# Optimization experiments

Hardware: AMD Instinct MI355X
Metric: run time of the kernel (lower is better)

Reference implementation:

```python
import jax, jax.numpy as jnp
import numpy as np

N, E, IN_DIM, HID = 50000, 800000, 512, 256
EPS = 1e-5


def _gat_layer(x, W, a_src, a_dst, b, src, dst, n, heads, ch):
    # x: [N, F_in] -> h: [N, H, C]
    h = (x @ W).reshape(n, heads, ch)
    alpha_src = jnp.sum(h * a_src, axis=-1)  # [N, H]
    alpha_dst = jnp.sum(h * a_dst, axis=-1)  # [N, H]
    e = jax.nn.leaky_relu(alpha_src[src] + alpha_dst[dst], negative_slope=0.2)  # [E', H]
    # segment softmax over incoming edges of each destination node
    m = jax.ops.segment_max(e, dst, num_segments=n)  # [N, H]
    ex = jnp.exp(e - m[dst])
    den = jax.ops.segment_sum(ex, dst, num_segments=n)  # [N, H]
    alpha = ex / den[dst]
    out = jax.ops.segment_sum(alpha[:, :, None] * h[src], dst, num_segments=n)  # [N, H, C]
    return out.reshape(n, heads * ch) + b


def _layer_norm(x, w, b):
    mu = jnp.mean(x, axis=-1, keepdims=True)
    var = jnp.mean(jnp.square(x - mu), axis=-1, keepdims=True)
    return (x - mu) * jax.lax.rsqrt(var + EPS) * w + b


def setup_inputs() -> dict:
    key = jax.random.key(0)
    ks = jax.random.split(key, 16)
    d = {}
    d['x'] = jax.random.normal(ks[0], (N, IN_DIM), dtype=jnp.float32)
    d['edge_index'] = jax.random.randint(ks[1], (2, E), 0, N, dtype=jnp.int32)
    s = 0.05
    # layer 0: GATConv(512, 64, heads=4)
    d['W0'] = jax.random.normal(ks[2], (IN_DIM, HID), dtype=jnp.float32) * s
    d['as0'] = jax.random.normal(ks[3], (4, 64), dtype=jnp.float32) * s
    d['ad0'] = jax.random.normal(ks[4], (4, 64), dtype=jnp.float32) * s
    d['b0'] = jnp.zeros((HID,), dtype=jnp.float32)
    d['lnw0'] = jnp.ones((HID,), dtype=jnp.float32)
    d['lnb0'] = jnp.zeros((HID,), dtype=jnp.float32)
    # layer 1: GATConv(256, 64, heads=4)
    d['W1'] = jax.random.normal(ks[5], (HID, HID), dtype=jnp.float32) * s
    d['as1'] = jax.random.normal(ks[6], (4, 64), dtype=jnp.float32) * s
    d['ad1'] = jax.random.normal(ks[7], (4, 64), dtype=jnp.float32) * s
    d['b1'] = jnp.zeros((HID,), dtype=jnp.float32)
    d['lnw1'] = jnp.ones((HID,), dtype=jnp.float32)
    d['lnb1'] = jnp.zeros((HID,), dtype=jnp.float32)
    # layer 2: GATConv(256, 256, heads=1)
    d['W2'] = jax.random.normal(ks[8], (HID, HID), dtype=jnp.float32) * s
    d['as2'] = jax.random.normal(ks[9], (1, HID), dtype=jnp.float32) * s
    d['ad2'] = jax.random.normal(ks[10], (1, HID), dtype=jnp.float32) * s
    d['b2'] = jnp.zeros((HID,), dtype=jnp.float32)
    d['lnw2'] = jnp.ones((HID,), dtype=jnp.float32)
    d['lnb2'] = jnp.zeros((HID,), dtype=jnp.float32)
    return d


def reference(x, edge_index, W0, as0, ad0, b0, lnw0, lnb0,
              W1, as1, ad1, b1, lnw1, lnb1,
              W2, as2, ad2, b2, lnw2, lnb2):
    n = x.shape[0]
    loop = jnp.arange(n, dtype=edge_index.dtype)
    src = jnp.concatenate([edge_index[0], loop])  # PyG add_self_loops=True
    dst = jnp.concatenate([edge_index[1], loop])
    h = _gat_layer(x, W0, as0, ad0, b0, src, dst, n, 4, 64)
    h = jax.nn.elu(_layer_norm(h, lnw0, lnb0))
    h = _gat_layer(h, W1, as1, ad1, b1, src, dst, n, 4, 64)
    h = jax.nn.elu(_layer_norm(h, lnw1, lnb1))
    h = _gat_layer(h, W2, as2, ad2, b2, src, dst, n, 1, HID)
    h = jax.nn.elu(_layer_norm(h, lnw2, lnb2))
    return h
```

## Files before the change

### kernel.cpp

```cpp
#include <hip/hip_runtime.h>

#define HID 256
#define EPSV 1e-5f
#define ASTR 72
#define BSTR 40

typedef __bf16 bf16x8 __attribute__((ext_vector_type(8)));
typedef float  floatx4 __attribute__((ext_vector_type(4)));

static __device__ __forceinline__ ushort f2bf(float f) {
  union { float f; unsigned int i; } c; c.f = f;
  unsigned int u = c.i;
  u += 0x7FFFu + ((u >> 16) & 1u);
  return (ushort)(u >> 16);
}
static __device__ __forceinline__ float bf2f(ushort u) {
  union { unsigned int i; float f; } c; c.i = ((unsigned int)u) << 16; return c.f;
}

__global__ void count_kernel(const int* __restrict__ ei, int* __restrict__ deg, int E, int tot) {
  int i = blockIdx.x * blockDim.x + threadIdx.x;
  if (i < tot) {
    int dst = (i < E) ? ei[E + i] : (i - E);
    atomicAdd(&deg[dst], 1);
  }
}

__global__ void scanA_kernel(const int* __restrict__ deg, int* __restrict__ incl,
                             int* __restrict__ sums, int n) {
  __shared__ int buf[1024];
  const int t = threadIdx.x;
  const int i = blockIdx.x * 1024 + t;
  int x = (i < n) ? deg[i] : 0;
  buf[t] = x;
  __syncthreads();
  for (int off = 1; off < 1024; off <<= 1) {
    int v = (t >= off) ? buf[t - off] : 0;
    __syncthreads();
    buf[t] += v;
    __syncthreads();
  }
  if (i < n) incl[i] = buf[t];
  if (t == 1023) sums[blockIdx.x] = buf[1023];
}

__global__ void scanB_kernel(int* __restrict__ sums, int* __restrict__ offs, int nblk) {
  __shared__ int buf[256];
  const int t = threadIdx.x;
  int x = (t < nblk) ? sums[t] : 0;
  buf[t] = x;
  __syncthreads();
  for (int off = 1; off < 256; off <<= 1) {
    int v = (t >= off) ? buf[t - off] : 0;
    __syncthreads();
    buf[t] += v;
    __syncthreads();
  }
  if (t < nblk) offs[t] = buf[t] - x;
  if (t == nblk) offs[nblk] = buf[nblk - 1];
}

__global__ void scanC_kernel(const int* __restrict__ deg, const int* __restrict__ incl,
                             const int* __restrict__ offs, int* __restrict__ rp,
                             int* __restrict__ cur, int n, int nblk) {
  const int i = blockIdx.x * 1024 + threadIdx.x;
  if (i < n) {
    int v = offs[blockIdx.x] + incl[i] - deg[i];
    rp[i] = v;
    cur[i] = v;
  }
  if (i == 0) rp[n] = offs[nblk];
}

__global__ void scatter_kernel(const int* __restrict__ ei, int* __restrict__ cur,
                               int* __restrict__ csr, int E, int tot) {
  int i = blockIdx.x * blockDim.x + threadIdx.x;
  if (i < tot) {
    int src = (i < E) ? ei[i] : (i - E);
    int dst = (i < E) ? ei[E + i] : (i - E);
    int pos = atomicAdd(&cur[dst], 1);
    csr[pos] = src;
  }
}

__global__ void transpose_kernel(const float* __restrict__ W, ushort* __restrict__ Wt, int K) {
  int i = blockIdx.x * blockDim.x + threadIdx.x;
  if (i < K * 256) {
    int k = i >> 8, m = i & 255;
    Wt[m * K + k] = f2bf(W[i]);
  }
}

static __device__ __forceinline__ void alpha_epilogue(
    const floatx4 (&acc)[4][4], const float* __restrict__ avs,
    const float* __restrict__ avd, float* __restrict__ asrc,
    float* __restrict__ adst, int row0, int col0, int wm, int wn,
    int quad, int m16, int H, int nrows) {
  float sv[4], dv[4];
  #pragma unroll
  for (int j = 0; j < 4; j++) {
    int col = col0 + wn + j * 16 + m16;
    sv[j] = avs[col];
    dv[j] = avd[col];
  }
  const int hd = (col0 + wn) >> 6;
  #pragma unroll
  for (int i = 0; i < 4; i++) {
    #pragma unroll
    for (int r = 0; r < 4; r++) {
      int row = row0 + wm + i * 16 + quad * 4 + r;
      float s = 0.f, d = 0.f;
      #pragma unroll
      for (int j = 0; j < 4; j++) {
        s = fmaf(acc[i][j][r], sv[j], s);
        d = fmaf(acc[i][j][r], dv[j], d);
      }
      #pragma unroll
      for (int o = 1; o < 16; o <<= 1) { s += __shfl_xor(s, o); d += __shfl_xor(d, o); }
      if (m16 == 0 && row < nrows) {
        if (H == 4) {
          asrc[row * 4 + hd] = s;
          adst[row * 4 + hd] = d;
        } else {
          atomicAdd(&asrc[row], s);
          atomicAdd(&adst[row], d);
        }
      }
    }
  }
}

__global__ __launch_bounds__(256) void gemm_kernel(
    const float* __restrict__ A, const ushort* __restrict__ Bt,
    ushort* __restrict__ hb, const float* __restrict__ avs,
    const float* __restrict__ avd, float* __restrict__ asrc,
    float* __restrict__ adst, int nrows, int K) {
  __shared__ ushort At[128 * ASTR];
  __shared__ ushort Bs[128 * BSTR];
  const int tid  = threadIdx.x;
  const int lane = tid & 63;
  const int wave = tid >> 6;
  const int quad = lane >> 4;
  const int m16  = lane & 15;
  const int row0 = blockIdx.x * 128;
  const int col0 = blockIdx.y * 128;
  const int wm = (wave >> 1) * 64;
  const int wn = (wave & 1) * 64;

  floatx4 acc[4][4];
  #pragma unroll
  for (int i = 0; i < 4; i++)
    #pragma unroll
    for (int j = 0; j < 4; j++) acc[i][j] = (floatx4){0.f, 0.f, 0.f, 0.f};

  const int arow = tid >> 3;
  const int acol = (tid & 7) * 4;
  const int brow = tid >> 2;
  const int bcol = (tid & 3) * 8;

  for (int k0 = 0; k0 < K; k0 += 32) {
    #pragma unroll
    for (int i = 0; i < 4; i++) {
      int r = arow + 32 * i;
      int ar = min(row0 + r, nrows - 1);
      floatx4 v = *(const floatx4*)(A + (size_t)ar * K + k0 + acol);
      union { ushort us[4]; unsigned long long u64; } ph, pl;
      #pragma unroll
      for (int j = 0; j < 4; j++) {
        ushort hi = f2bf(v[j]);
        ph.us[j] = hi;
        pl.us[j] = f2bf(v[j] - bf2f(hi));
      }
      *(unsigned long long*)&At[r * ASTR + acol]      = ph.u64;
      *(unsigned long long*)&At[r * ASTR + 32 + acol] = pl.u64;
    }
    #pragma unroll
    for (int i = 0; i < 2; i++) {
      int r = brow + 64 * i;
      *(int4*)&Bs[r * BSTR + bcol] =
          *(const int4*)(Bt + (size_t)(col0 + r) * K + k0 + bcol);
    }
    __syncthreads();
    bf16x8 bfr[4];
    #pragma unroll
    for (int j = 0; j < 4; j++)
      bfr[j] = *(const bf16x8*)&Bs[(wn + j * 16 + m16) * BSTR + quad * 8];
    #pragma unroll
    for (int p = 0; p < 2; p++) {
      bf16x8 af[4];
      #pragma unroll
      for (int i = 0; i < 4; i++)
        af[i] = *(const bf16x8*)&At[(wm + i * 16 + m16) * ASTR + p * 32 + quad * 8];
      #pragma unroll
      for (int i = 0; i < 4; i++)
        #pragma unroll
        for (int j = 0; j < 4; j++)
          acc[i][j] = __builtin_amdgcn_mfma_f32_16x16x32_bf16(af[i], bfr[j], acc[i][j], 0, 0, 0);
    }
    __syncthreads();
  }
  #pragma unroll
  for (int i = 0; i < 4; i++) {
    int rbase = row0 + wm + i * 16 + quad * 4;
    #pragma unroll
    for (int j = 0; j < 4; j++) {
      int col = col0 + wn + j * 16 + m16;
      #pragma unroll
      for (int r = 0; r < 4; r++) {
        int row = rbase + r;
        if (row < nrows) hb[(size_t)row * HID + col] = f2bf(acc[i][j][r]);
      }
    }
  }
  alpha_epilogue(acc, avs, avd, asrc, adst, row0, col0, wm, wn, quad, m16, 4, nrows);
}

__global__ __launch_bounds__(256) void gemm_packed_kernel(
    const ushort* __restrict__ A, const ushort* __restrict__ Bt,
    ushort* __restrict__ hb, const float* __restrict__ avs,
    const float* __restrict__ avd, float* __restrict__ asrc,
    float* __restrict__ adst, int nrows, int H) {
  __shared__ ushort At[128 * BSTR];
  __shared__ ushort Bs[128 * BSTR];
  const int tid  = threadIdx.x;
  const int lane = tid & 63;
  const int wave = tid >> 6;
  const int quad = lane >> 4;
  const int m16  = lane & 15;
  const int row0 = blockIdx.x * 128;
  const int col0 = blockIdx.y * 128;
  const int wm = (wave >> 1) * 64;
  const int wn = (wave & 1) * 64;

  floatx4 acc[4][4];
  #pragma unroll
  for (int i = 0; i < 4; i++)
    #pragma unroll
    for (int j = 0; j < 4; j++) acc[i][j] = (floatx4){0.f, 0.f, 0.f, 0.f};

  const int srow = tid >> 2;
  const int scol = (tid & 3) * 8;

  for (int k0 = 0; k0 < 512; k0 += 32) {
    const int kb = k0 & 255;
    #pragma unroll
    for (int i = 0; i < 2; i++) {
      int r = srow + 64 * i;
      int ar = min(row0 + r, nrows - 1);
      *(int4*)&At[r * BSTR + scol] = *(const int4*)(A + (size_t)ar * 512 + k0 + scol);
      *(int4*)&Bs[r * BSTR + scol] = *(const int4*)(Bt + (size_t)(col0 + r) * 256 + kb + scol);
    }
    __syncthreads();
    bf16x8 af[4], bfr[4];
    #pragma unroll
    for (int j = 0; j < 4; j++)
      bfr[j] = *(const bf16x8*)&Bs[(wn + j * 16 + m16) * BSTR + quad * 8];
    #pragma unroll
    for (int i = 0; i < 4; i++)
      af[i] = *(const bf16x8*)&At[(wm + i * 16 + m16) * BSTR + quad * 8];
    #pragma unroll
    for (int i = 0; i < 4; i++)
      #pragma unroll
      for (int j = 0; j < 4; j++)
        acc[i][j] = __builtin_amdgcn_mfma_f32_16x16x32_bf16(af[i], bfr[j], acc[i][j], 0, 0, 0);
    __syncthreads();
  }
  #pragma unroll
  for (int i = 0; i < 4; i++) {
    int rbase = row0 + wm + i * 16 + quad * 4;
    #pragma unroll
    for (int j = 0; j < 4; j++) {
      int col = col0 + wn + j * 16 + m16;
      #pragma unroll
      for (int r = 0; r < 4; r++) {
        int row = rbase + r;
        if (row < nrows) hb[(size_t)row * HID + col] = f2bf(acc[i][j][r]);
      }
    }
  }
  alpha_epilogue(acc, avs, avd, asrc, adst, row0, col0, wm, wn, quad, m16, H, nrows);
}

__global__ __launch_bounds__(256) void agg_ln_kernel(
    const ushort* __restrict__ hb, const float* __restrict__ asrc,
    const float* __restrict__ adst, const int* __restrict__ rp,
    const int* __restrict__ csr,
    const float* __restrict__ bias, const float* __restrict__ lnw,
    const float* __restrict__ lnb, ushort* __restrict__ apk,
    float* __restrict__ fout, int H, int n) {
  __shared__ float2 exs[4][64];
  const int t = threadIdx.x;
  const int w = t >> 6, lane = t & 63;
  const int nid = blockIdx.x * 4 + w;
  if (nid >= n) return;
  const int CH = (H == 4) ? 16 : 64;
  const int jj = lane & (CH - 1);
  const int hh = (H == 4) ? (lane >> 4) : 0;
  const int ch = 4 * lane;
  const float ad = adst[nid * H + hh];
  const int beg = rp[nid], end = rp[nid + 1];
  const char* hbase = (const char*)hb + ch * 2;
  float den = 0.f;
  float a0 = 0.f, a1 = 0.f, a2 = 0.f, a3 = 0.f;
  float b0 = 0.f, b1 = 0.f, b2 = 0.f, b3 = 0.f;
  float c0_ = 0.f, c1 = 0.f, c2 = 0.f, c3 = 0.f;
  float d0_ = 0.f, d1 = 0.f, d2 = 0.f, d3 = 0.f;

  int snext = 0;
  {
    int cnt0 = min(CH, end - beg);
    if (lane < cnt0) snext = csr[beg + lane];
  }

  for (int c0 = beg; c0 < end; c0 += CH) {
    const int cnt = min(CH, end - c0);
    int s = snext;
    const int nc0 = c0 + CH;
    if (nc0 < end) {
      int ncnt = min(CH, end - nc0);
      if (lane < ncnt) snext = csr[nc0 + lane];
    }
    s = __shfl(s, jj);
    float ex = 0.f;
    if (jj < cnt) {
      float e = asrc[s * H + hh] + ad;
      e = (e > 0.f) ? e : 0.2f * e;
      ex = __expf(fminf(e, 60.f));
    }
    exs[w][lane] = make_float2(ex, __int_as_float(s << 9));
    float dsum = ex;
    #pragma unroll
    for (int o = 32; o > 0; o >>= 1)
      if (o < CH) dsum += __shfl_xor(dsum, o);
    den += dsum;
    const float2* exw = &exs[w][hh * CH];
    int j = 0;
    for (; j + 4 <= cnt; j += 4) {
      float2 q0 = exw[j];
      float2 q1 = exw[j + 1];
      float2 q2 = exw[j + 2];
      float2 q3 = exw[j + 3];
      uint2 u0 = *(const uint2*)(hbase + __float_as_int(q0.y));
      uint2 u1 = *(const uint2*)(hbase + __float_as_int(q1.y));
      uint2 u2 = *(const uint2*)(hbase + __float_as_int(q2.y));
      uint2 u3 = *(const uint2*)(hbase + __float_as_int(q3.y));
      a0 = fmaf(q0.x, __uint_as_float(u0.x << 16), a0);
      a1 = fmaf(q0.x, __uint_as_float(u0.x & 0xffff0000u), a1);
      a2 = fmaf(q0.x, __uint_as_float(u0.y << 16), a2);
      a3 = fmaf(q0.x, __uint_as_float(u0.y & 0xffff0000u), a3);
      b0 = fmaf(q1.x, __uint_as_float(u1.x << 16), b0);
      b1 = fmaf(q1.x, __uint_as_float(u1.x & 0xffff0000u), b1);
      b2 = fmaf(q1.x, __uint_as_float(u1.y << 16), b2);
      b3 = fmaf(q1.x, __uint_as_float(u1.y & 0xffff0000u), b3);
      c0_ = fmaf(q2.x, __uint_as_float(u2.x << 16), c0_);
      c1 = fmaf(q2.x, __uint_as_float(u2.x & 0xffff0000u), c1);
      c2 = fmaf(q2.x, __uint_as_float(u2.y << 16), c2);
      c3 = fmaf(q2.x, __uint_as_float(u2.y & 0xffff0000u), c3);
      d0_ = fmaf(q3.x, __uint_as_float(u3.x << 16), d0_);
      d1 = fmaf(q3.x, __uint_as_float(u3.x & 0xffff0000u), d1);
      d2 = fmaf(q3.x, __uint_as_float(u3.y << 16), d2);
      d3 = fmaf(q3.x, __uint_as_float(u3.y & 0xffff0000u), d3);
    }
    for (; j < cnt; ++j) {
      float2 q0 = exw[j];
      uint2 u0 = *(const uint2*)(hbase + __float_as_int(q0.y));
      a0 = fmaf(q0.x, __uint_as_float(u0.x << 16), a0);
      a1 = fmaf(q0.x, __uint_as_float(u0.x & 0xffff0000u), a1);
      a2 = fmaf(q0.x, __uint_as_float(u0.y << 16), a2);
      a3 = fmaf(q0.x, __uint_as_float(u0.y & 0xffff0000u), a3);
    }
  }
  a0 += b0 + c0_ + d0_;
  a1 += b1 + c1 + d1;
  a2 += b2 + c2 + d2;
  a3 += b3 + c3 + d3;

  const float inv = 1.f / den;
  const floatx4 bia = *(const floatx4*)(bias + ch);
  float v0 = a0 * inv + bia[0];
  float v1 = a1 * inv + bia[1];
  float v2 = a2 * inv + bia[2];
  float v3 = a3 * inv + bia[3];
  float r1 = v0 + v1 + v2 + v3;
  #pragma unroll
  for (int o = 32; o > 0; o >>= 1) r1 += __shfl_xor(r1, o);
  float mu = r1 * (1.f / HID);
  float e0 = v0 - mu, e1 = v1 - mu, e2 = v2 - mu, e3 = v3 - mu;
  float r2 = e0 * e0 + e1 * e1 + e2 * e2 + e3 * e3;
  #pragma unroll
  for (int o = 32; o > 0; o >>= 1) r2 += __shfl_xor(r2, o);
  float rstd = rsqrtf(r2 * (1.f / HID) + EPSV);
  const floatx4 wv = *(const floatx4*)(lnw + ch);
  const floatx4 bv = *(const floatx4*)(lnb + ch);
  float y0 = e0 * rstd * wv[0] + bv[0];
  float y1 = e1 * rstd * wv[1] + bv[1];
  float y2 = e2 * rstd * wv[2] + bv[2];
  float y3 = e3 * rstd * wv[3] + bv[3];
  float o0 = (y0 > 0.f) ? y0 : expm1f(y0);
  float o1 = (y1 > 0.f) ? y1 : expm1f(y1);
  float o2 = (y2 > 0.f) ? y2 : expm1f(y2);
  float o3 = (y3 > 0.f) ? y3 : expm1f(y3);
  if (apk) {
    union { ushort us[4]; unsigned long long u64; } ph, pl;
    ushort h0 = f2bf(o0), h1 = f2bf(o1), h2 = f2bf(o2), h3 = f2bf(o3);
    ph.us[0] = h0; ph.us[1] = h1; ph.us[2] = h2; ph.us[3] = h3;
    pl.us[0] = f2bf(o0 - bf2f(h0)); pl.us[1] = f2bf(o1 - bf2f(h1));
    pl.us[2] = f2bf(o2 - bf2f(h2)); pl.us[3] = f2bf(o3 - bf2f(h3));
    *(unsigned long long*)(apk + (size_t)nid * 512 + ch)       = ph.u64;
    *(unsigned long long*)(apk + (size_t)nid * 512 + 256 + ch) = pl.u64;
  } else {
    floatx4 ov; ov[0] = o0; ov[1] = o1; ov[2] = o2; ov[3] = o3;
    *(floatx4*)(fout + (size_t)nid * HID + ch) = ov;
  }
}

extern "C" void kernel_launch(void* const* d_in, const int* in_sizes, int n_in,
                              void* d_out, int out_size, void* d_ws, size_t ws_size,
                              hipStream_t stream) {
  const float* x  = (const float*)d_in[0];
  const int*   ei = (const int*)d_in[1];
  const float* Wm[3]  = {(const float*)d_in[2], (const float*)d_in[8],  (const float*)d_in[14]};
  const float* Avs[3] = {(const float*)d_in[3], (const float*)d_in[9],  (const float*)d_in[15]};
  const float* Avd[3] = {(const float*)d_in[4], (const float*)d_in[10], (const float*)d_in[16]};
  const float* Bia[3] = {(const float*)d_in[5], (const float*)d_in[11], (const float*)d_in[17]};
  const float* Lnw[3] = {(const float*)d_in[6], (const float*)d_in[12], (const float*)d_in[18]};
  const float* Lnb[3] = {(const float*)d_in[7], (const float*)d_in[13], (const float*)d_in[19]};
  const int n = in_sizes[0] / 512;
  const int E = in_sizes[1] / 2;
  const int tot = E + n;
  const int nblk = (n + 1023) / 1024;

  char* p = (char*)d_ws;
  ushort* hb   = (ushort*)p; p += (size_t)n * HID * 2;
  ushort* apk  = (ushort*)p; p += (size_t)n * 512 * 2;
  ushort* Wt   = (ushort*)p; p += 256 * 512 * 2;
  float*  asrc = (float*)p;  p += (size_t)n * 4 * 4;
  float*  adst = (float*)p;  p += (size_t)n * 4 * 4;
  int* rp   = (int*)p; p += (size_t)(n + 1) * 4;
  int* cur  = (int*)p; p += (size_t)n * 4;
  int* csr  = (int*)p; p += (size_t)tot * 4;
  int* deg  = (int*)p; p += (size_t)n * 4;
  int* incl = (int*)p; p += (size_t)n * 4;
  int* sums = (int*)p; p += (size_t)(nblk + 1) * 4;
  int* offs = (int*)p; p += (size_t)(nblk + 1) * 4;

  hipMemsetAsync(deg, 0, (size_t)n * 4, stream);
  count_kernel<<<(tot + 255) / 256, 256, 0, stream>>>(ei, deg, E, tot);
  scanA_kernel<<<nblk, 1024, 0, stream>>>(deg, incl, sums, n);
  scanB_kernel<<<1, 256, 0, stream>>>(sums, offs, nblk);
  scanC_kernel<<<nblk, 1024, 0, stream>>>(deg, incl, offs, rp, cur, n, nblk);
  scatter_kernel<<<(tot + 255) / 256, 256, 0, stream>>>(ei, cur, csr, E, tot);

  const int KB[3] = {512, 256, 256};
  const int HH[3] = {4, 4, 1};
  dim3 gg((n + 127) / 128, 2);
  for (int l = 0; l < 3; l++) {
    transpose_kernel<<<(KB[l] * 256 + 255) / 256, 256, 0, stream>>>(Wm[l], Wt, KB[l]);
    if (HH[l] == 1) {
      hipMemsetAsync(asrc, 0, (size_t)n * 4, stream);
      hipMemsetAsync(adst, 0, (size_t)n * 4, stream);
    }
    if (l == 0)
      gemm_kernel<<<gg, 256, 0, stream>>>(x, Wt, hb, Avs[l], Avd[l], asrc, adst, n, 512);
    else
      gemm_packed_kernel<<<gg, 256, 0, stream>>>(apk, Wt, hb, Avs[l], Avd[l], asrc, adst, n, HH[l]);
    agg_ln_kernel<<<(n + 3) / 4, 256, 0, stream>>>(
        hb, asrc, adst, rp, csr, Bia[l], Lnw[l], Lnb[l],
        (l < 2) ? apk : (ushort*)nullptr,
        (l == 2) ? (float*)d_out : (float*)nullptr, HH[l], n);
  }
}
```

Baseline: 641.7 us.

## Prefetch GEMM tiles into registers, tile weight transpose, drop H=1 atomics

Both GEMM kernels now load the next K-slice of A and B from global memory into registers while MFMAs run on the current shared-memory tile, which hides global load latency behind compute. The fp32 to bf16 hi/lo split uses byte permutes and truncation instead of rounding. The weight transpose goes through a shared-memory tile so its accesses are coalesced. For the single-head layer, the per-column-block alpha partial sums are stored as four separate values and added in the aggregation kernel, which removes atomics and two memsets at the cost of an extra vector load per edge.

```diff
diff --git a/kernel.cpp b/kernel.cpp
--- a/kernel.cpp
+++ b/kernel.cpp
@@ -83,19 +83,26 @@
   }
 }
 
-__global__ void transpose_kernel(const float* __restrict__ W, ushort* __restrict__ Wt, int K) {
-  int i = blockIdx.x * blockDim.x + threadIdx.x;
-  if (i < K * 256) {
-    int k = i >> 8, m = i & 255;
-    Wt[m * K + k] = f2bf(W[i]);
-  }
+__global__ __launch_bounds__(256) void transpose_kernel(
+    const float* __restrict__ W, ushort* __restrict__ Wt, int K) {
+  __shared__ ushort tile[32][33];
+  const int tx = threadIdx.x & 31, ty = threadIdx.x >> 5;
+  const int bm = blockIdx.x * 32;
+  const int bk = blockIdx.y * 32;
+  #pragma unroll
+  for (int yy = ty; yy < 32; yy += 8)
+    tile[tx][yy] = f2bf(W[(size_t)(bk + yy) * 256 + bm + tx]);
+  __syncthreads();
+  #pragma unroll
+  for (int yy = ty; yy < 32; yy += 8)
+    Wt[(size_t)(bm + yy) * K + bk + tx] = tile[yy][tx];
 }
 
 static __device__ __forceinline__ void alpha_epilogue(
     const floatx4 (&acc)[4][4], const float* __restrict__ avs,
     const float* __restrict__ avd, float* __restrict__ asrc,
     float* __restrict__ adst, int row0, int col0, int wm, int wn,
-    int quad, int m16, int H, int nrows) {
+    int quad, int m16, int nrows) {
   float sv[4], dv[4];
   #pragma unroll
   for (int j = 0; j < 4; j++) {
@@ -103,7 +110,7 @@
     sv[j] = avs[col];
     dv[j] = avd[col];
   }
-  const int hd = (col0 + wn) >> 6;
+  const int idx = (col0 + wn) >> 6;
   #pragma unroll
   for (int i = 0; i < 4; i++) {
     #pragma unroll
@@ -118,13 +125,8 @@
       #pragma unroll
       for (int o = 1; o < 16; o <<= 1) { s += __shfl_xor(s, o); d += __shfl_xor(d, o); }
       if (m16 == 0 && row < nrows) {
-        if (H == 4) {
-          asrc[row * 4 + hd] = s;
-          adst[row * 4 + hd] = d;
-        } else {
-          atomicAdd(&asrc[row], s);
-          atomicAdd(&adst[row], d);
-        }
+        asrc[row * 4 + idx] = s;
+        adst[row * 4 + idx] = d;
       }
     }
   }
@@ -158,29 +160,53 @@
   const int brow = tid >> 2;
   const int bcol = (tid & 3) * 8;
 
+  const float* pa[4];
+  const ushort* pb[2];
+  #pragma unroll
+  for (int i = 0; i < 4; i++) {
+    int r = arow + 32 * i;
+    int ar = min(row0 + r, nrows - 1);
+    pa[i] = A + (size_t)ar * K + acol;
+  }
+  #pragma unroll
+  for (int i = 0; i < 2; i++)
+    pb[i] = Bt + (size_t)(col0 + brow + 64 * i) * K + bcol;
+
+  floatx4 rA[4];
+  int4 rB[2];
+  #pragma unroll
+  for (int i = 0; i < 4; i++) rA[i] = *(const floatx4*)pa[i];
+  #pragma unroll
+  for (int i = 0; i < 2; i++) rB[i] = *(const int4*)pb[i];
+
   for (int k0 = 0; k0 < K; k0 += 32) {
     #pragma unroll
     for (int i = 0; i < 4; i++) {
       int r = arow + 32 * i;
-      int ar = min(row0 + r, nrows - 1);
-      floatx4 v = *(const floatx4*)(A + (size_t)ar * K + k0 + acol);
-      union { ushort us[4]; unsigned long long u64; } ph, pl;
-      #pragma unroll
-      for (int j = 0; j < 4; j++) {
-        ushort hi = f2bf(v[j]);
-        ph.us[j] = hi;
-        pl.us[j] = f2bf(v[j] - bf2f(hi));
-      }
-      *(unsigned long long*)&At[r * ASTR + acol]      = ph.u64;
-      *(unsigned long long*)&At[r * ASTR + 32 + acol] = pl.u64;
-    }
-    #pragma unroll
-    for (int i = 0; i < 2; i++) {
-      int r = brow + 64 * i;
-      *(int4*)&Bs[r * BSTR + bcol] =
-          *(const int4*)(Bt + (size_t)(col0 + r) * K + k0 + bcol);
-    }
-    __syncthreads();
+      floatx4 v = rA[i];
+      unsigned u0 = __float_as_uint(v[0]), u1 = __float_as_uint(v[1]);
+      unsigned u2 = __float_as_uint(v[2]), u3 = __float_as_uint(v[3]);
+      unsigned ph0 = __builtin_amdgcn_perm(u1, u0, 0x07060302u);
+      unsigned ph1 = __builtin_amdgcn_perm(u3, u2, 0x07060302u);
+      float l0 = v[0] - __uint_as_float(u0 & 0xffff0000u);
+      float l1 = v[1] - __uint_as_float(u1 & 0xffff0000u);
+      float l2 = v[2] - __uint_as_float(u2 & 0xffff0000u);
+      float l3 = v[3] - __uint_as_float(u3 & 0xffff0000u);
+      unsigned pl0 = __builtin_amdgcn_perm(__float_as_uint(l1), __float_as_uint(l0), 0x07060302u);
+      unsigned pl1 = __builtin_amdgcn_perm(__float_as_uint(l3), __float_as_uint(l2), 0x07060302u);
+      *(uint2*)&At[r * ASTR + acol]      = make_uint2(ph0, ph1);
+      *(uint2*)&At[r * ASTR + 32 + acol] = make_uint2(pl0, pl1);
+    }
+    #pragma unroll
+    for (int i = 0; i < 2; i++)
+      *(int4*)&Bs[(brow + 64 * i) * BSTR + bcol] = rB[i];
+    __syncthreads();
+    if (k0 + 32 < K) {
+      #pragma unroll
+      for (int i = 0; i < 4; i++) rA[i] = *(const floatx4*)(pa[i] + k0 + 32);
+      #pragma unroll
+      for (int i = 0; i < 2; i++) rB[i] = *(const int4*)(pb[i] + k0 + 32);
+    }
     bf16x8 bfr[4];
     #pragma unroll
     for (int j = 0; j < 4; j++)
@@ -212,14 +238,14 @@
       }
     }
   }
-  alpha_epilogue(acc, avs, avd, asrc, adst, row0, col0, wm, wn, quad, m16, 4, nrows);
+  alpha_epilogue(acc, avs, avd, asrc, adst, row0, col0, wm, wn, quad, m16, nrows);
 }
 
 __global__ __launch_bounds__(256) void gemm_packed_kernel(
     const ushort* __restrict__ A, const ushort* __restrict__ Bt,
     ushort* __restrict__ hb, const float* __restrict__ avs,
     const float* __restrict__ avd, float* __restrict__ asrc,
-    float* __restrict__ adst, int nrows, int H) {
+    float* __restrict__ adst, int nrows) {
   __shared__ ushort At[128 * BSTR];
   __shared__ ushort Bs[128 * BSTR];
   const int tid  = threadIdx.x;
@@ -241,16 +267,36 @@
   const int srow = tid >> 2;
   const int scol = (tid & 3) * 8;
 
+  const ushort* pa[2];
+  const ushort* pb[2];
+  #pragma unroll
+  for (int i = 0; i < 2; i++) {
+    int r = srow + 64 * i;
+    int ar = min(row0 + r, nrows - 1);
+    pa[i] = A + (size_t)ar * 512 + scol;
+    pb[i] = Bt + (size_t)(col0 + r) * 256 + scol;
+  }
+
+  int4 rA[2], rB[2];
+  #pragma unroll
+  for (int i = 0; i < 2; i++) { rA[i] = *(const int4*)pa[i]; rB[i] = *(const int4*)pb[i]; }
+
   for (int k0 = 0; k0 < 512; k0 += 32) {
-    const int kb = k0 & 255;
     #pragma unroll
     for (int i = 0; i < 2; i++) {
       int r = srow + 64 * i;
-      int ar = min(row0 + r, nrows - 1);
-      *(int4*)&At[r * BSTR + scol] = *(const int4*)(A + (size_t)ar * 512 + k0 + scol);
-      *(int4*)&Bs[r * BSTR + scol] = *(const int4*)(Bt + (size_t)(col0 + r) * 256 + kb + scol);
-    }
-    __syncthreads();
+      *(int4*)&At[r * BSTR + scol] = rA[i];
+      *(int4*)&Bs[r * BSTR + scol] = rB[i];
+    }
+    __syncthreads();
+    if (k0 + 32 < 512) {
+      int kn = k0 + 32, kbn = kn & 255;
+      #pragma unroll
+      for (int i = 0; i < 2; i++) {
+        rA[i] = *(const int4*)(pa[i] + kn);
+        rB[i] = *(const int4*)(pb[i] + kbn);
+      }
+    }
     bf16x8 af[4], bfr[4];
     #pragma unroll
     for (int j = 0; j < 4; j++)
@@ -278,7 +324,7 @@
       }
     }
   }
-  alpha_epilogue(acc, avs, avd, asrc, adst, row0, col0, wm, wn, quad, m16, H, nrows);
+  alpha_epilogue(acc, avs, avd, asrc, adst, row0, col0, wm, wn, quad, m16, nrows);
 }
 
 __global__ __launch_bounds__(256) void agg_ln_kernel(
@@ -297,7 +343,13 @@
   const int jj = lane & (CH - 1);
   const int hh = (H == 4) ? (lane >> 4) : 0;
   const int ch = 4 * lane;
-  const float ad = adst[nid * H + hh];
+  float ad;
+  if (H == 4) {
+    ad = adst[nid * 4 + hh];
+  } else {
+    floatx4 t4 = *(const floatx4*)(adst + nid * 4);
+    ad = t4[0] + t4[1] + t4[2] + t4[3];
+  }
   const int beg = rp[nid], end = rp[nid + 1];
   const char* hbase = (const char*)hb + ch * 2;
   float den = 0.f;
@@ -323,7 +375,13 @@
     s = __shfl(s, jj);
     float ex = 0.f;
     if (jj < cnt) {
-      float e = asrc[s * H + hh] + ad;
+      float e;
+      if (H == 4) {
+        e = asrc[s * 4 + hh] + ad;
+      } else {
+        floatx4 t4 = *(const floatx4*)(asrc + s * 4);
+        e = t4[0] + t4[1] + t4[2] + t4[3] + ad;
+      }
       e = (e > 0.f) ? e : 0.2f * e;
       ex = __expf(fminf(e, 60.f));
     }
@@ -455,15 +513,12 @@
   const int HH[3] = {4, 4, 1};
   dim3 gg((n + 127) / 128, 2);
   for (int l = 0; l < 3; l++) {
-    transpose_kernel<<<(KB[l] * 256 + 255) / 256, 256, 0, stream>>>(Wm[l], Wt, KB[l]);
-    if (HH[l] == 1) {
-      hipMemsetAsync(asrc, 0, (size_t)n * 4, stream);
-      hipMemsetAsync(adst, 0, (size_t)n * 4, stream);
-    }
+    dim3 tg(8, KB[l] / 32);
+    transpose_kernel<<<tg, 256, 0, stream>>>(Wm[l], Wt, KB[l]);
     if (l == 0)
       gemm_kernel<<<gg, 256, 0, stream>>>(x, Wt, hb, Avs[l], Avd[l], asrc, adst, n, 512);
     else
-      gemm_packed_kernel<<<gg, 256, 0, stream>>>(apk, Wt, hb, Avs[l], Avd[l], asrc, adst, n, HH[l]);
+      gemm_packed_kernel<<<gg, 256, 0, stream>>>(apk, Wt, hb, Avs[l], Avd[l], asrc, adst, n);
     agg_ln_kernel<<<(n + 3) / 4, 256, 0, stream>>>(
         hb, asrc, adst, rp, csr, Bia[l], Lnw[l], Lnb[l],
         (l < 2) ? apk : (ushort*)nullptr,
```

Result: slower. 747.2 us (+16.4%).
